# Optimization experiments

Hardware: AMD Instinct MI355X
Metric: run time of the kernel (lower is better)

Reference implementation:

```python
import jax, jax.numpy as jnp
import numpy as np

N_NODES = 50000
N_EDGES = 1600000
N_FEAT = 128
HIDDEN = 128
N_GRAPHS = 64
N_CLASSES = 10
N_REGS = 1


def setup_inputs() -> dict:
    key = jax.random.key(0)
    ks = jax.random.split(key, 16)
    inp = {
        "x": jax.random.normal(ks[0], (N_NODES, N_FEAT), dtype=jnp.float32),
        "edge_index": jax.random.randint(ks[1], (2, N_EDGES), 0, N_NODES, dtype=jnp.int32),
        "batch": jnp.sort(jax.random.randint(ks[2], (N_NODES,), 0, N_GRAPHS, dtype=jnp.int32)),
        # GCNConv layer params (PyG: linear without bias applied first, bias added after aggregation)
        "w0": jax.random.normal(ks[3], (N_FEAT, HIDDEN), dtype=jnp.float32) * 0.05,
        "b0": jax.random.normal(ks[4], (HIDDEN,), dtype=jnp.float32) * 0.05,
        "w1": jax.random.normal(ks[5], (HIDDEN, HIDDEN), dtype=jnp.float32) * 0.05,
        "b1": jax.random.normal(ks[6], (HIDDEN,), dtype=jnp.float32) * 0.05,
        "w2": jax.random.normal(ks[7], (HIDDEN, HIDDEN), dtype=jnp.float32) * 0.05,
        "b2": jax.random.normal(ks[8], (HIDDEN,), dtype=jnp.float32) * 0.05,
        # heads
        "wc": jax.random.normal(ks[9], (HIDDEN, N_CLASSES), dtype=jnp.float32) * 0.05,
        "bc": jax.random.normal(ks[10], (N_CLASSES,), dtype=jnp.float32) * 0.05,
        "wr": jax.random.normal(ks[11], (HIDDEN, N_REGS), dtype=jnp.float32) * 0.05,
        "br": jax.random.normal(ks[12], (N_REGS,), dtype=jnp.float32) * 0.05,
    }
    return inp


def _gcn_layer(x, src, dst, w, b, deg_inv_sqrt, deg_inv):
    # x: [N, Din] -> [N, Dout]. GCNConv: D^-1/2 (A+I) D^-1/2 (x W) + b
    h = x @ w  # [N, Dout]
    coef = (deg_inv_sqrt[src] * deg_inv_sqrt[dst])[:, None]  # [E, 1]
    agg = jax.ops.segment_sum(h[src] * coef, dst, num_segments=x.shape[0])
    agg = agg + h * deg_inv[:, None]  # self-loop term: deg^-1 * h
    return agg + b


def reference(x, edge_index, batch, w0, b0, w1, b1, w2, b2, wc, bc, wr, br):
    src, dst = edge_index[0], edge_index[1]
    n = x.shape[0]
    # degrees include self-loop weight 1 (PyG gcn_norm with edge_weight=1)
    deg = jax.ops.segment_sum(jnp.ones(src.shape, x.dtype), dst, num_segments=n) + 1.0
    deg_inv_sqrt = deg ** -0.5
    deg_inv = 1.0 / deg

    h = _gcn_layer(x, src, dst, w0, b0, deg_inv_sqrt, deg_inv)
    h = _gcn_layer(jax.nn.elu(h), src, dst, w1, b1, deg_inv_sqrt, deg_inv)
    h = _gcn_layer(jax.nn.elu(h), src, dst, w2, b2, deg_inv_sqrt, deg_inv)

    # global mean pool over graphs
    sums = jax.ops.segment_sum(h, batch, num_segments=N_GRAPHS)  # [G, H]
    cnt = jax.ops.segment_sum(jnp.ones((n,), h.dtype), batch, num_segments=N_GRAPHS)
    pooled = sums / jnp.maximum(cnt, 1.0)[:, None]

    cls_out = pooled @ wc + bc
    reg_out = pooled @ wr + br
    return (pooled, cls_out, reg_out)
```

## Files before the change

kernel.cpp:

```cpp
#include <hip/hip_runtime.h>
#include <hip/hip_fp16.h>
#include <math.h>

#define N_NODES   50000
#define N_EDGES   1600000
#define NF        128
#define N_GRAPHS  64
#define N_CLASSES 10

#define NBK       391
#define BK_SHIFT  7
#define BK_NODES  128
#define SLAB      5120
#define CHUNK     4096
#define NCHUNKS   ((N_EDGES + CHUNK - 1) / CHUNK)
#define NODES_PER_BLK 8
#define NBLK_AGG  (N_NODES / NODES_PER_BLK)

typedef _Float16 half8 __attribute__((ext_vector_type(8)));
typedef float f32x4 __attribute__((ext_vector_type(4)));

__global__ void k_init(int* __restrict__ bucket_cur, float* __restrict__ sums,
                       const float* __restrict__ w0, const float* __restrict__ w1,
                       const float* __restrict__ w2, _Float16* __restrict__ wf) {
    int b = blockIdx.x, t = threadIdx.x;
    if (b < 3) {
        const float* W = (b == 0) ? w0 : (b == 1) ? w1 : w2;
        _Float16* dst = wf + (size_t)b * NF * NF;
        for (int idx = t; idx < NF * NF; idx += 256) {
            int k = idx >> 7, n = idx & 127;
            int nt = n >> 4, kc = k >> 5, quad = (k >> 3) & 3, j = k & 7;
            int lane = quad * 16 + (n & 15);
            dst[((nt * 4 + kc) * 64 + lane) * 8 + j] = (_Float16)W[idx];
        }
    } else {
        int i = (b - 3) * 256 + t;
        if (i < NBK) bucket_cur[i] = i * SLAB;
        if (i < N_GRAPHS * NF) sums[i] = 0.f;
    }
}

__global__ __launch_bounds__(256) void k_bscatter(const int* __restrict__ src,
                                                  const int* __restrict__ dst,
                                                  int* __restrict__ bucket_cur,
                                                  int* __restrict__ pairs) {
    __shared__ int h[NBK], rb[NBK], c2[NBK];
    int t = threadIdx.x;
    for (int i = t; i < NBK; i += 256) { h[i] = 0; c2[i] = 0; }
    __syncthreads();
    int base = blockIdx.x * CHUNK;
    int end = min(base + CHUNK, N_EDGES);
    for (int e = base + t; e < end; e += 256)
        atomicAdd(&h[dst[e] >> BK_SHIFT], 1);
    __syncthreads();
    for (int i = t; i < NBK; i += 256)
        rb[i] = h[i] ? atomicAdd(&bucket_cur[i], h[i]) : 0;
    __syncthreads();
    for (int e = base + t; e < end; e += 256) {
        int d = dst[e];
        int b = d >> BK_SHIFT;
        int k = atomicAdd(&c2[b], 1);
        pairs[rb[b] + k] = (src[e] << BK_SHIFT) | (d & (BK_NODES - 1));
    }
}

__global__ __launch_bounds__(512) void k_bfill(const int* __restrict__ pairs,
                                               const int* __restrict__ bucket_cur,
                                               int* __restrict__ row_start,
                                               int* __restrict__ row_end,
                                               float* __restrict__ dis,
                                               int* __restrict__ csr_src) {
    __shared__ int cnt[BK_NODES];
    __shared__ int cur[BK_NODES];
    __shared__ int ts[512];
    int b = blockIdx.x, t = threadIdx.x;
    int node_base = b << BK_SHIFT;
    int lo = b * SLAB, hi = bucket_cur[b];

    if (t < BK_NODES) cnt[t] = 0;
    __syncthreads();
    for (int e = lo + t; e < hi; e += 512)
        atomicAdd(&cnt[pairs[e] & (BK_NODES - 1)], 1);
    __syncthreads();

    int a = (t < BK_NODES) ? cnt[t] : 0;
    ts[t] = a;
    __syncthreads();
    for (int off = 1; off < BK_NODES; off <<= 1) {
        int y = (t >= off) ? ts[t - off] : 0;
        __syncthreads();
        ts[t] += y;
        __syncthreads();
    }
    int row = lo + ts[t] - a;
    if (t < BK_NODES) {
        cur[t] = row;
        int n = node_base + t;
        if (n < N_NODES) {
            row_start[n] = row;
            row_end[n]   = row + a;
            dis[n] = rsqrtf((float)(a + 1));
        }
    }
    __syncthreads();

    for (int e = lo + t; e < hi; e += 512) {
        int p = pairs[e];
        int pos = atomicAdd(&cur[p & (BK_NODES - 1)], 1);
        csr_src[pos] = p >> BK_SHIFT;
    }
}

template <bool ELU, bool FP32IN>
__global__ __launch_bounds__(256) void k_gemm(const void* __restrict__ Xv,
                                              const _Float16* __restrict__ WF,
                                              const float* __restrict__ dis,
                                              __half* __restrict__ H) {
    __shared__ _Float16 xs[64 * 136];
    const _Float16* Xh = (const _Float16*)Xv;
    const float*    Xf = (const float*)Xv;
    int t = threadIdx.x;
    int row0 = blockIdx.x * 64;
#pragma unroll
    for (int i = 0; i < 4; i++) {
        int f = i * 256 + t;
        int r = f >> 4, c = (f & 15) * 8;
        int gr = row0 + r;
        half8 v = {};
        if (gr < N_NODES) {
            if (FP32IN) {
                float4 v0 = *(const float4*)&Xf[(size_t)gr * NF + c];
                float4 v1 = *(const float4*)&Xf[(size_t)gr * NF + c + 4];
                v[0] = (_Float16)v0.x; v[1] = (_Float16)v0.y;
                v[2] = (_Float16)v0.z; v[3] = (_Float16)v0.w;
                v[4] = (_Float16)v1.x; v[5] = (_Float16)v1.y;
                v[6] = (_Float16)v1.z; v[7] = (_Float16)v1.w;
            } else {
                v = *(const half8*)&Xh[(size_t)gr * NF + c];
            }
        }
        if (ELU) {
#pragma unroll
            for (int j = 0; j < 8; j++) {
                float xv = (float)v[j];
                v[j] = (_Float16)(xv > 0.f ? xv : (expf(xv) - 1.f));
            }
        }
        *(half8*)&xs[r * 136 + c] = v;
    }
    __syncthreads();

    int w = t >> 6;
    int lane = t & 63;
    int m = lane & 15, quad = lane >> 4;

    half8 a[4];
#pragma unroll
    for (int kc = 0; kc < 4; kc++)
        a[kc] = *(const half8*)&xs[(w * 16 + m) * 136 + kc * 32 + quad * 8];

    f32x4 acc[8];
#pragma unroll
    for (int nt = 0; nt < 8; nt++) {
        f32x4 c4 = {0.f, 0.f, 0.f, 0.f};
#pragma unroll
        for (int kc = 0; kc < 4; kc++) {
            half8 bf = *(const half8*)&WF[((nt * 4 + kc) * 64 + lane) * 8];
            c4 = __builtin_amdgcn_mfma_f32_16x16x32_f16(a[kc], bf, c4, 0, 0, 0);
        }
        acc[nt] = c4;
    }

    __syncthreads();
#pragma unroll
    for (int reg = 0; reg < 4; reg++) {
        int r = w * 16 + quad * 4 + reg;
        int gr = row0 + r;
        float ds = (gr < N_NODES) ? dis[gr] : 0.f;
#pragma unroll
        for (int nt = 0; nt < 8; nt++)
            xs[r * 136 + nt * 16 + m] = (_Float16)(ds * acc[nt][reg]);
    }
    __syncthreads();
#pragma unroll
    for (int i = 0; i < 4; i++) {
        int f = i * 256 + t;
        int r = f >> 4, c = (f & 15) * 8;
        int gr = row0 + r;
        if (gr < N_NODES)
            *(half8*)&H[(size_t)gr * NF + c] = *(const half8*)&xs[r * 136 + c];
    }
}

template <bool POOL>
__global__ __launch_bounds__(256) void k_agg(const __half* __restrict__ H,
                                             const float* __restrict__ bias,
                                             const int* __restrict__ row_start,
                                             const int* __restrict__ row_end,
                                             const int* __restrict__ csr_src,
                                             const float* __restrict__ dis,
                                             const int* __restrict__ batch,
                                             float* __restrict__ partial,
                                             float* __restrict__ sums,
                                             void* __restrict__ outv) {
    __shared__ float pacc[NF];
    const uint2* H4 = (const uint2*)H;
    int t = threadIdx.x;
    int lane = t & 63;
    int node = blockIdx.x * NODES_PER_BLK + (t >> 6) * 2 + (lane >> 5);
    int l    = lane & 31;
    int c    = l * 4;
    if (POOL) {
        if (t < NF) pacc[t] = 0.f;
        __syncthreads();
    }
    float o0 = 0.f, o1 = 0.f, o2 = 0.f, o3 = 0.f;
    bool active = node < N_NODES;
    if (active) {
        int rs = row_start[node], re = row_end[node];
        float a0 = 0.f, a1 = 0.f, a2 = 0.f, a3 = 0.f;
        int e = rs;
        for (; e + 7 < re; e += 8) {
            uint2 v[8];
#pragma unroll
            for (int j = 0; j < 8; j++) {
                int s = csr_src[e + j];
                v[j] = H4[(size_t)s * 32 + l];
            }
#pragma unroll
            for (int j = 0; j < 8; j++) {
                float2 lo = __half22float2(*(__half2*)&v[j].x);
                float2 hi = __half22float2(*(__half2*)&v[j].y);
                a0 += lo.x; a1 += lo.y; a2 += hi.x; a3 += hi.y;
            }
        }
        for (; e < re; e++) {
            int s = csr_src[e];
            uint2 v = H4[(size_t)s * 32 + l];
            float2 lo = __half22float2(*(__half2*)&v.x);
            float2 hi = __half22float2(*(__half2*)&v.y);
            a0 += lo.x; a1 += lo.y; a2 += hi.x; a3 += hi.y;
        }
        {
            uint2 v = H4[(size_t)node * 32 + l];
            float2 lo = __half22float2(*(__half2*)&v.x);
            float2 hi = __half22float2(*(__half2*)&v.y);
            a0 += lo.x; a1 += lo.y; a2 += hi.x; a3 += hi.y;
        }
        float di = dis[node];
        float4 bv = *(const float4*)&bias[c];
        o0 = a0 * di + bv.x; o1 = a1 * di + bv.y;
        o2 = a2 * di + bv.z; o3 = a3 * di + bv.w;
        if (!POOL) {
            uint2 o;
            *(__half2*)&o.x = __floats2half2_rn(o0, o1);
            *(__half2*)&o.y = __floats2half2_rn(o2, o3);
            ((uint2*)outv)[(size_t)node * 32 + l] = o;
        }
    }
    if (POOL) {
        int first = blockIdx.x * NODES_PER_BLK;
        int last  = min(first + NODES_PER_BLK - 1, N_NODES - 1);
        int g0 = batch[first], g7 = batch[last];
        if (g0 == g7) {
            if (active) {
                atomicAdd(&pacc[c + 0], o0);
                atomicAdd(&pacc[c + 1], o1);
                atomicAdd(&pacc[c + 2], o2);
                atomicAdd(&pacc[c + 3], o3);
            }
            __syncthreads();
            if (t < NF) partial[(size_t)blockIdx.x * NF + t] = pacc[t];
        } else if (active) {
            int g = batch[node];
            atomicAdd(&sums[g * NF + c + 0], o0);
            atomicAdd(&sums[g * NF + c + 1], o1);
            atomicAdd(&sums[g * NF + c + 2], o2);
            atomicAdd(&sums[g * NF + c + 3], o3);
        }
    }
}

__global__ void k_head(const float* __restrict__ sums, const float* __restrict__ partial,
                       const int* __restrict__ batch,
                       const float* __restrict__ wc, const float* __restrict__ bc,
                       const float* __restrict__ wr, const float* __restrict__ br,
                       float* __restrict__ out) {
    __shared__ float p[128];
    __shared__ int sh[2];
    int g = blockIdx.x, c = threadIdx.x;
    if (c < 2) {
        int tgt = g + c;
        int lo = 0, hi = N_NODES;
        while (lo < hi) { int m = (lo + hi) >> 1; if (batch[m] < tgt) lo = m + 1; else hi = m; }
        sh[c] = lo;
    }
    __syncthreads();
    int s0 = sh[0], s1 = sh[1];
    float acc = sums[g * NF + c];
    int js = (s0 + NODES_PER_BLK - 1) / NODES_PER_BLK;
    int je = s1 / NODES_PER_BLK;
    for (int j = js; j < je; j++) acc += partial[(size_t)j * NF + c];
    float cnt = (float)max(s1 - s0, 1);
    float pv = acc / cnt;
    p[c] = pv;
    out[g * NF + c] = pv;
    __syncthreads();
    if (c < N_CLASSES) {
        float d = bc[c];
        for (int k = 0; k < NF; k++) d += p[k] * wc[k * N_CLASSES + c];
        out[N_GRAPHS * NF + g * N_CLASSES + c] = d;
    }
    if (c == N_CLASSES) {
        float d = br[0];
        for (int k = 0; k < NF; k++) d += p[k] * wr[k];
        out[N_GRAPHS * NF + N_GRAPHS * N_CLASSES + g] = d;
    }
}

extern "C" void kernel_launch(void* const* d_in, const int* in_sizes, int n_in,
                              void* d_out, int out_size, void* d_ws, size_t ws_size,
                              hipStream_t stream) {
    const float* x     = (const float*)d_in[0];
    const int*   ei    = (const int*)d_in[1];
    const int*   batch = (const int*)d_in[2];
    const float* w0 = (const float*)d_in[3];
    const float* b0 = (const float*)d_in[4];
    const float* w1 = (const float*)d_in[5];
    const float* b1 = (const float*)d_in[6];
    const float* w2 = (const float*)d_in[7];
    const float* b2 = (const float*)d_in[8];
    const float* wc = (const float*)d_in[9];
    const float* bc = (const float*)d_in[10];
    const float* wr = (const float*)d_in[11];
    const float* br = (const float*)d_in[12];
    const int* srcp = ei;
    const int* dstp = ei + N_EDGES;
    float* out = (float*)d_out;

    char* ws = (char*)d_ws;
    size_t off = 0;
    auto alloc = [&](size_t bytes) -> void* {
        void* p = ws + off;
        off = (off + bytes + 255) & ~(size_t)255;
        return p;
    };
    int*      row_start  = (int*)alloc(N_NODES * 4);
    int*      row_end    = (int*)alloc(N_NODES * 4);
    int*      bucket_cur = (int*)alloc(NBK * 4);
    float*    dis        = (float*)alloc(N_NODES * 4);
    int*      csr_src    = (int*)alloc((size_t)NBK * SLAB * 4);
    __half*   Hbuf       = (__half*)alloc((size_t)N_NODES * NF * 2);
    _Float16* Ah         = (_Float16*)alloc((size_t)N_NODES * NF * 2);
    _Float16* wf         = (_Float16*)alloc((size_t)3 * NF * NF * 2);
    float*    sums       = (float*)alloc(N_GRAPHS * NF * 4);
    float*    partial    = (float*)alloc((size_t)NBLK_AGG * NF * 4);
    (void)ws_size;
    int* pairs = (int*)Hbuf;

    k_init<<<35, 256, 0, stream>>>(bucket_cur, sums, w0, w1, w2, wf);
    k_bscatter<<<NCHUNKS, 256, 0, stream>>>(srcp, dstp, bucket_cur, pairs);
    k_bfill<<<NBK, 512, 0, stream>>>(pairs, bucket_cur, row_start, row_end, dis, csr_src);

    const int gemm_grid = (N_NODES + 63) / 64;

    k_gemm<false, true><<<gemm_grid, 256, 0, stream>>>(x, wf, dis, Hbuf);
    k_agg<false><<<NBLK_AGG, 256, 0, stream>>>(Hbuf, b0, row_start, row_end, csr_src, dis, batch, partial, sums, Ah);
    k_gemm<true, false><<<gemm_grid, 256, 0, stream>>>(Ah, wf + NF * NF, dis, Hbuf);
    k_agg<false><<<NBLK_AGG, 256, 0, stream>>>(Hbuf, b1, row_start, row_end, csr_src, dis, batch, partial, sums, Ah);
    k_gemm<true, false><<<gemm_grid, 256, 0, stream>>>(Ah, wf + 2 * NF * NF, dis, Hbuf);
    k_agg<true><<<NBLK_AGG, 256, 0, stream>>>(Hbuf, b2, row_start, row_end, csr_src, dis, batch, partial, sums, nullptr);

    k_head<<<N_GRAPHS, 128, 0, stream>>>(sums, partial, batch, wc, bc, wr, br, out);
}
```

Measured before the change: 396.4 us.

## Sort CSR neighbors by source tile and pool per wave without LDS atomics

The bucket fill now counts edges per (destination node, source-index tile of 8192 nodes) and prefix-sums over 1024 bins. Within each row, neighbor sources come out grouped by source range, which should give the gather in the aggregation kernels better cache locality. The final pooling drops the shared-memory atomic accumulation and block barrier. Each wave instead combines its two nodes with a cross-lane shuffle and writes one partial row per wave, and the head kernel reads these at wave granularity. The cost is a larger partial buffer, more head-kernel summation, and a longer scan in the fill kernel.

```diff
diff --git a/kernel.cpp b/kernel.cpp
--- a/kernel.cpp
+++ b/kernel.cpp
@@ -16,6 +16,9 @@
 #define NCHUNKS   ((N_EDGES + CHUNK - 1) / CHUNK)
 #define NODES_PER_BLK 8
 #define NBLK_AGG  (N_NODES / NODES_PER_BLK)
+#define N_WAVES   (N_NODES / 2)
+#define TILE_SHIFT 13
+#define NTILE     8
 
 typedef _Float16 half8 __attribute__((ext_vector_type(8)));
 typedef float f32x4 __attribute__((ext_vector_type(4)));
@@ -70,44 +73,53 @@
                                                int* __restrict__ row_end,
                                                float* __restrict__ dis,
                                                int* __restrict__ csr_src) {
-    __shared__ int cnt[BK_NODES];
-    __shared__ int cur[BK_NODES];
+    __shared__ int cnt[BK_NODES * NTILE];
+    __shared__ int cur[BK_NODES * NTILE];
+    __shared__ int pos[BK_NODES * NTILE + 1];
     __shared__ int ts[512];
     int b = blockIdx.x, t = threadIdx.x;
     int node_base = b << BK_SHIFT;
     int lo = b * SLAB, hi = bucket_cur[b];
 
-    if (t < BK_NODES) cnt[t] = 0;
-    __syncthreads();
-    for (int e = lo + t; e < hi; e += 512)
-        atomicAdd(&cnt[pairs[e] & (BK_NODES - 1)], 1);
-    __syncthreads();
-
-    int a = (t < BK_NODES) ? cnt[t] : 0;
-    ts[t] = a;
-    __syncthreads();
-    for (int off = 1; off < BK_NODES; off <<= 1) {
+    cnt[t] = 0; cnt[t + 512] = 0;
+    __syncthreads();
+    for (int e = lo + t; e < hi; e += 512) {
+        int p = pairs[e];
+        atomicAdd(&cnt[(p & (BK_NODES - 1)) * NTILE + (p >> (BK_SHIFT + TILE_SHIFT))], 1);
+    }
+    __syncthreads();
+
+    int a0 = cnt[2 * t], a1 = cnt[2 * t + 1];
+    ts[t] = a0 + a1;
+    __syncthreads();
+    for (int off = 1; off < 512; off <<= 1) {
         int y = (t >= off) ? ts[t - off] : 0;
         __syncthreads();
         ts[t] += y;
         __syncthreads();
     }
-    int row = lo + ts[t] - a;
+    int ex = lo + ts[t] - (a0 + a1);
+    pos[2 * t] = ex;       cur[2 * t] = ex;
+    pos[2 * t + 1] = ex + a0; cur[2 * t + 1] = ex + a0;
+    if (t == 511) pos[1024] = lo + ts[511];
+    __syncthreads();
+
     if (t < BK_NODES) {
-        cur[t] = row;
         int n = node_base + t;
         if (n < N_NODES) {
-            row_start[n] = row;
-            row_end[n]   = row + a;
-            dis[n] = rsqrtf((float)(a + 1));
+            int r0 = pos[t * NTILE], r1 = pos[(t + 1) * NTILE];
+            row_start[n] = r0;
+            row_end[n]   = r1;
+            dis[n] = rsqrtf((float)(r1 - r0 + 1));
         }
     }
     __syncthreads();
 
     for (int e = lo + t; e < hi; e += 512) {
         int p = pairs[e];
-        int pos = atomicAdd(&cur[p & (BK_NODES - 1)], 1);
-        csr_src[pos] = p >> BK_SHIFT;
+        int idx = (p & (BK_NODES - 1)) * NTILE + (p >> (BK_SHIFT + TILE_SHIFT));
+        int ps = atomicAdd(&cur[idx], 1);
+        csr_src[ps] = p >> BK_SHIFT;
     }
 }
 
@@ -200,20 +212,15 @@
                                              const int* __restrict__ csr_src,
                                              const float* __restrict__ dis,
                                              const int* __restrict__ batch,
-                                             float* __restrict__ partial,
+                                             float* __restrict__ partialw,
                                              float* __restrict__ sums,
                                              void* __restrict__ outv) {
-    __shared__ float pacc[NF];
     const uint2* H4 = (const uint2*)H;
     int t = threadIdx.x;
     int lane = t & 63;
     int node = blockIdx.x * NODES_PER_BLK + (t >> 6) * 2 + (lane >> 5);
     int l    = lane & 31;
     int c    = l * 4;
-    if (POOL) {
-        if (t < NF) pacc[t] = 0.f;
-        __syncthreads();
-    }
     float o0 = 0.f, o1 = 0.f, o2 = 0.f, o3 = 0.f;
     bool active = node < N_NODES;
     if (active) {
@@ -259,18 +266,16 @@
         }
     }
     if (POOL) {
-        int first = blockIdx.x * NODES_PER_BLK;
-        int last  = min(first + NODES_PER_BLK - 1, N_NODES - 1);
-        int g0 = batch[first], g7 = batch[last];
-        if (g0 == g7) {
-            if (active) {
-                atomicAdd(&pacc[c + 0], o0);
-                atomicAdd(&pacc[c + 1], o1);
-                atomicAdd(&pacc[c + 2], o2);
-                atomicAdd(&pacc[c + 3], o3);
-            }
-            __syncthreads();
-            if (t < NF) partial[(size_t)blockIdx.x * NF + t] = pacc[t];
+        int node0 = blockIdx.x * NODES_PER_BLK + (t >> 6) * 2;
+        int wave_id = node0 >> 1;
+        float s0 = o0 + __shfl_down(o0, 32);
+        float s1 = o1 + __shfl_down(o1, 32);
+        float s2 = o2 + __shfl_down(o2, 32);
+        float s3 = o3 + __shfl_down(o3, 32);
+        int n1 = min(node0 + 1, N_NODES - 1);
+        if (batch[node0] == batch[n1]) {
+            if (lane < 32)
+                *(float4*)&partialw[(size_t)wave_id * NF + c] = make_float4(s0, s1, s2, s3);
         } else if (active) {
             int g = batch[node];
             atomicAdd(&sums[g * NF + c + 0], o0);
@@ -281,7 +286,7 @@
     }
 }
 
-__global__ void k_head(const float* __restrict__ sums, const float* __restrict__ partial,
+__global__ void k_head(const float* __restrict__ sums, const float* __restrict__ partialw,
                        const int* __restrict__ batch,
                        const float* __restrict__ wc, const float* __restrict__ bc,
                        const float* __restrict__ wr, const float* __restrict__ br,
@@ -298,9 +303,9 @@
     __syncthreads();
     int s0 = sh[0], s1 = sh[1];
     float acc = sums[g * NF + c];
-    int js = (s0 + NODES_PER_BLK - 1) / NODES_PER_BLK;
-    int je = s1 / NODES_PER_BLK;
-    for (int j = js; j < je; j++) acc += partial[(size_t)j * NF + c];
+    int js = (s0 + 1) >> 1;
+    int je = s1 >> 1;
+    for (int j = js; j < je; j++) acc += partialw[(size_t)j * NF + c];
     float cnt = (float)max(s1 - s0, 1);
     float pv = acc / cnt;
     p[c] = pv;
@@ -354,7 +359,7 @@
     _Float16* Ah         = (_Float16*)alloc((size_t)N_NODES * NF * 2);
     _Float16* wf         = (_Float16*)alloc((size_t)3 * NF * NF * 2);
     float*    sums       = (float*)alloc(N_GRAPHS * NF * 4);
-    float*    partial    = (float*)alloc((size_t)NBLK_AGG * NF * 4);
+    float*    partialw   = (float*)alloc((size_t)N_WAVES * NF * 4);
     (void)ws_size;
     int* pairs = (int*)Hbuf;
 
@@ -365,11 +370,11 @@
     const int gemm_grid = (N_NODES + 63) / 64;
 
     k_gemm<false, true><<<gemm_grid, 256, 0, stream>>>(x, wf, dis, Hbuf);
-    k_agg<false><<<NBLK_AGG, 256, 0, stream>>>(Hbuf, b0, row_start, row_end, csr_src, dis, batch, partial, sums, Ah);
+    k_agg<false><<<NBLK_AGG, 256, 0, stream>>>(Hbuf, b0, row_start, row_end, csr_src, dis, batch, partialw, sums, Ah);
     k_gemm<true, false><<<gemm_grid, 256, 0, stream>>>(Ah, wf + NF * NF, dis, Hbuf);
-    k_agg<false><<<NBLK_AGG, 256, 0, stream>>>(Hbuf, b1, row_start, row_end, csr_src, dis, batch, partial, sums, Ah);
+    k_agg<false><<<NBLK_AGG, 256, 0, stream>>>(Hbuf, b1, row_start, row_end, csr_src, dis, batch, partialw, sums, Ah);
     k_gemm<true, false><<<gemm_grid, 256, 0, stream>>>(Ah, wf + 2 * NF * NF, dis, Hbuf);
-    k_agg<true><<<NBLK_AGG, 256, 0, stream>>>(Hbuf, b2, row_start, row_end, csr_src, dis, batch, partial, sums, nullptr);
-
-    k_head<<<N_GRAPHS, 128, 0, stream>>>(sums, partial, batch, wc, bc, wr, br, out);
-}
+    k_agg<true><<<NBLK_AGG, 256, 0, stream>>>(Hbuf, b2, row_start, row_end, csr_src, dis, batch, partialw, sums, nullptr);
+
+    k_head<<<N_GRAPHS, 128, 0, stream>>>(sums, partialw, batch, wc, bc, wr, br, out);
+}
```

Result: slower. 442.4 us (+11.6%).
